# Optimization experiments

Measured on AMD Instinct MI355X. Metric: run time of the kernel, lower is better.

## Reference

```python
import jax, jax.numpy as jnp
import numpy as np

B, T, D, H, HS = 4, 1024, 1024, 16, 64
DW, DA, DG, DV = 64, 64, 128, 32
DM = H * HS  # == D here
EPS = 1e-5
DECAY_C = -0.606531  # -exp(-0.5)


def setup_inputs() -> dict:
    key = jax.random.key(0)
    ks = jax.random.split(key, 24)
    n = lambda k, s: jax.random.normal(k, s, dtype=jnp.float32)
    w = lambda k, s: n(k, s) * (1.0 / np.sqrt(s[0]))
    return dict(
        current=n(ks[0], (B, T, D)),
        prev=n(ks[1], (B, T, D)),
        v_first=n(ks[2], (B, T, DM)),
        rwkvag=jax.random.uniform(ks[3], (6, D), dtype=jnp.float32),
        rw_W=w(ks[4], (D, D)),
        w1=w(ks[5], (D, DW)), w2=w(ks[6], (DW, DM)), w2_b=n(ks[7], (DM,)) * 0.1,
        kw_W=w(ks[8], (D, DM)), vw_W=w(ks[9], (D, DM)),
        a1=w(ks[10], (D, DA)), a2=w(ks[11], (DA, DM)), a2_b=n(ks[12], (DM,)) * 0.1,
        v1=w(ks[13], (D, DV)), v2=w(ks[14], (DV, DM)), v2_b=n(ks[15], (DM,)) * 0.1,
        g1=w(ks[16], (D, DG)), g2=w(ks[17], (DG, DM)), g2_b=n(ks[18], (DM,)) * 0.1,
        k_k=jnp.ones((DM,)), k_a=jax.random.uniform(ks[19], (DM,), dtype=jnp.float32),
        r_k=jnp.ones((DM,)),
        gn_scale=jnp.ones((DM,)), gn_bias=jnp.zeros((DM,)),
        out_W=w(ks[20], (DM, D)),
    )


def _add_heads(x):
    return x.reshape(x.shape[:-1] + (H, HS))


def reference(current, prev, v_first, rwkvag, rw_W, w1, w2, w2_b, kw_W, vw_W,
              a1, a2, a2_b, v1, v2, v2_b, g1, g2, g2_b,
              k_k, k_a, r_k, gn_scale, gn_bias, out_W):
    diff = prev - current
    # per-channel token-shift mixing for the 6 branches: (B,T,6,D)
    x6 = current[..., None, :] + rwkvag * diff[..., None, :]
    xr, xw, xk, xv, xa, xg = (x6[..., i, :] for i in range(6))

    r = xr @ rw_W
    wl = jnp.tanh(xw @ w1) @ w2 + w2_b          # w-LoRA (tanh, bias_post)
    k = xk @ kw_W
    v = xv @ vw_W
    a = jax.nn.sigmoid((xa @ a1) @ a2 + a2_b)   # a-LoRA (bias_post) + sigmoid
    g = jax.nn.sigmoid(xg @ g1) @ g2 + g2_b     # g-LoRA (sigmoid act)

    kk = _add_heads(k * k_k)
    kk = kk / jnp.linalg.norm(kk, axis=-1, keepdims=True)
    k = k * (1.0 + (a - 1.0) * k_a)
    v = v + (v_first - v) * jax.nn.sigmoid((xv @ v1) @ v2 + v2_b)
    wdec = jnp.exp(DECAY_C * jax.nn.sigmoid(wl))  # decay in (exp(-0.6065), 1)

    rk_sum = _add_heads(r * k * r_k).sum(-1, keepdims=True)  # (B,T,H,1)
    rh, wh, kh, vh = _add_heads(r), _add_heads(wdec), _add_heads(k), _add_heads(v)
    at = -kk
    bt = kk * _add_heads(a)

    def step(state, xs):
        rt, wt, ktt, vt, att, btt = xs  # each (B,H,HS)
        sa = jnp.einsum('bhvk,bhk->bhv', state, att)
        state = (state * wt[:, :, None, :]
                 + sa[..., None] * btt[:, :, None, :]
                 + vt[..., None] * ktt[:, :, None, :])
        y = jnp.einsum('bhvk,bhk->bhv', state, rt)
        return state, y

    xs = tuple(jnp.moveaxis(x, 1, 0) for x in (rh, wh, kh, vh, at, bt))
    state0 = jnp.zeros((B, H, HS, HS), dtype=current.dtype)
    state, ys = jax.lax.scan(step, state0, xs)
    out = jnp.moveaxis(ys, 0, 1)  # (B,T,H,HS)

    # GroupNorm with n_head groups (normalize within each head)
    mu = out.mean(-1, keepdims=True)
    var = out.var(-1, keepdims=True)
    outn = (out - mu) * jax.lax.rsqrt(var + EPS)
    outn = outn.reshape(B, T, DM) * gn_scale + gn_bias

    outn = outn + (rk_sum * vh).reshape(B, T, DM)
    y = (outn * g) @ out_W
    return y, state, v_first
```

## Files before the change

kernel.cpp:

```cpp
#include <hip/hip_runtime.h>
#include <math.h>

#define NT 4096
#define DD 1024
#define NH 16
#define HSZ 64
#define GN_EPS 1e-5f
#define DECAY_C -0.606531f

typedef __attribute__((ext_vector_type(8))) short short8;
typedef __attribute__((ext_vector_type(4))) float float4v;

#define GLB(p) ((const __attribute__((address_space(1))) void*)(p))
#define LDS(p) ((__attribute__((address_space(3))) void*)(p))

#define MEMFENCE asm volatile("" ::: "memory")

__device__ __forceinline__ float sigm(float x) { return 1.f / (1.f + __expf(-x)); }

__device__ __forceinline__ unsigned short f2bf(float f) {
    unsigned int u = __float_as_uint(f);
    u = (u + 0x7fffu + ((u >> 16) & 1u)) >> 16;
    return (unsigned short)u;
}
__device__ __forceinline__ float bf2f(unsigned short h) {
    return __uint_as_float(((unsigned int)h) << 16);
}

__device__ __forceinline__ float row_sum16(float x) {
    int t;
    t = __builtin_amdgcn_update_dpp(0, __float_as_int(x), 0x128, 0xF, 0xF, true);
    x += __int_as_float(t);
    t = __builtin_amdgcn_update_dpp(0, __float_as_int(x), 0x124, 0xF, 0xF, true);
    x += __int_as_float(t);
    t = __builtin_amdgcn_update_dpp(0, __float_as_int(x), 0x122, 0xF, 0xF, true);
    x += __int_as_float(t);
    t = __builtin_amdgcn_update_dpp(0, __float_as_int(x), 0x121, 0xF, 0xF, true);
    x += __int_as_float(t);
    return x;
}

__global__ __launch_bounds__(256)
void mix6(const float* __restrict__ cur, const float* __restrict__ prev,
          const float* __restrict__ lam,
          ushort* __restrict__ xrh, ushort* __restrict__ xrl,
          ushort* __restrict__ xwh, ushort* __restrict__ xwl,
          ushort* __restrict__ xkh, ushort* __restrict__ xkl,
          ushort* __restrict__ xvh, ushort* __restrict__ xvl,
          ushort* __restrict__ xah, ushort* __restrict__ xal,
          ushort* __restrict__ xgh, ushort* __restrict__ xgl)
{
    const int tok = blockIdx.x;
    const int d0 = threadIdx.x * 4;
    const size_t base = (size_t)tok * DD + d0;
    float4 c = *(const float4*)(cur + base);
    float4 p = *(const float4*)(prev + base);
    float dx = p.x - c.x, dy = p.y - c.y, dz = p.z - c.z, dw = p.w - c.w;
    ushort* hs[6] = {xrh, xwh, xkh, xvh, xah, xgh};
    ushort* ls[6] = {xrl, xwl, xkl, xvl, xal, xgl};
#pragma unroll
    for (int j = 0; j < 6; j++) {
        float4 l = *(const float4*)(lam + j * DD + d0);
        float m0 = c.x + l.x * dx;
        float m1 = c.y + l.y * dy;
        float m2 = c.z + l.z * dz;
        float m3 = c.w + l.w * dw;
        ushort4 h;
        h.x = f2bf(m0); h.y = f2bf(m1); h.z = f2bf(m2); h.w = f2bf(m3);
        *(ushort4*)(hs[j] + base) = h;
        ushort4 lo;
        lo.x = f2bf(m0 - bf2f(h.x));
        lo.y = f2bf(m1 - bf2f(h.y));
        lo.z = f2bf(m2 - bf2f(h.z));
        lo.w = f2bf(m3 - bf2f(h.w));
        *(ushort4*)(ls[j] + base) = lo;
    }
}

__global__ __launch_bounds__(256)
void transpose_pad(const float* __restrict__ W, ushort* __restrict__ Wh,
                   ushort* __restrict__ Wl, int K, int N)
{
    __shared__ float tile[32][33];
    const int bx = blockIdx.x * 32;
    const int by = blockIdx.y * 32;
    const int tx = threadIdx.x, ty = threadIdx.y;
#pragma unroll
    for (int i = 0; i < 32; i += 8) {
        float v = 0.f;
        if (bx + tx < N) v = W[(size_t)(by + ty + i) * N + bx + tx];
        tile[ty + i][tx] = v;
    }
    __syncthreads();
#pragma unroll
    for (int i = 0; i < 32; i += 8) {
        float v = tile[tx][ty + i];
        ushort h = f2bf(v);
        size_t o = (size_t)(bx + ty + i) * K + by + tx;
        Wh[o] = h;
        if (Wl) Wl[o] = f2bf(v - bf2f(h));
    }
}

#define SWZ(r) (((r) >> 1) & 3)

__global__ __launch_bounds__(256)
void gemm_mega1(const ushort* __restrict__ xrh, const ushort* __restrict__ xrl,
                const ushort* __restrict__ xwh, const ushort* __restrict__ xwl,
                const ushort* __restrict__ xkh, const ushort* __restrict__ xkl,
                const ushort* __restrict__ xvh, const ushort* __restrict__ xvl,
                const ushort* __restrict__ xah, const ushort* __restrict__ xal,
                const ushort* __restrict__ xgh, const ushort* __restrict__ xgl,
                const ushort* __restrict__ Bth, const ushort* __restrict__ Btl,
                float* __restrict__ r_buf, float* __restrict__ k_buf,
                float* __restrict__ v_buf,
                ushort* __restrict__ hwh, ushort* __restrict__ hwl,
                ushort* __restrict__ hah, ushort* __restrict__ hal,
                ushort* __restrict__ hvh, ushort* __restrict__ hvl,
                ushort* __restrict__ hgh, ushort* __restrict__ hgl)
{
    __shared__ ushort As[2][2][128 * 32];
    __shared__ ushort Bs[2][2][128 * 32];
    const int cb = blockIdx.y;
    const ushort* Ah; const ushort* Al;
    if (cb < 8)       { Ah = xrh; Al = xrl; }
    else if (cb < 16) { Ah = xkh; Al = xkl; }
    else if (cb < 24) { Ah = xvh; Al = xvl; }
    else if (cb == 24){ Ah = xwh; Al = xwl; }
    else if (cb == 25){ Ah = xah; Al = xal; }
    else if (cb == 26){ Ah = xvh; Al = xvl; }
    else              { Ah = xgh; Al = xgl; }

    const int tid = threadIdx.x;
    const int rowBase = blockIdx.x * 128;
    const int colBase = cb * 128;
    const int lane = tid & 63;
    const int wave = tid >> 6;
    const int wm = wave >> 1, wn = wave & 1;
    const int m15 = lane & 15, quad = lane >> 4;

    float4v zero4 = {0.f, 0.f, 0.f, 0.f};
    float4v acc[4][4];
#pragma unroll
    for (int i = 0; i < 4; i++)
#pragma unroll
        for (int j = 0; j < 4; j++) acc[i][j] = zero4;

#define STAGE1(kk, bb) do {                                                       \
    const int k0_ = (kk) * 32;                                                    \
    _Pragma("unroll")                                                             \
    for (int i_ = 0; i_ < 2; i_++) {                                              \
        int idx_ = i_ * 256 + tid;                                                \
        int r_ = idx_ >> 2, seg_ = idx_ & 3;                                      \
        int sg_ = seg_ ^ SWZ(r_);       \
        size_t aoff_ = (size_t)(rowBase + r_) * 1024 + k0_ + sg_ * 8;             \
        size_t boff_ = (size_t)(colBase + r_) * 1024 + k0_ + sg_ * 8;             \
        int dst_ = (i_ * 256 + (tid & ~63)) * 8;                                  \
        __builtin_amdgcn_global_load_lds(GLB(Ah + aoff_),  LDS(&As[bb][0][0] + dst_), 16, 0, 0); \
        __builtin_amdgcn_global_load_lds(GLB(Al + aoff_),  LDS(&As[bb][1][0] + dst_), 16, 0, 0); \
        __builtin_amdgcn_global_load_lds(GLB(Bth + boff_), LDS(&Bs[bb][0][0] + dst_), 16, 0, 0); \
        __builtin_amdgcn_global_load_lds(GLB(Btl + boff_), LDS(&Bs[bb][1][0] + dst_), 16, 0, 0); \
    }                                                                             \
} while (0)

    STAGE1(0, 0);
    STAGE1(1, 1);
    asm volatile("s_waitcnt vmcnt(8)" ::: "memory");
    __builtin_amdgcn_s_barrier();
    MEMFENCE;

    for (int kt = 0; kt < 32; kt++) {
        const int buf = kt & 1;

        short8 ah[4], bh[4], al[4], bl[4];
#pragma unroll
        for (int mi = 0; mi < 4; mi++) {
            int ra = wm * 64 + mi * 16 + m15;
            int cs = (quad ^ SWZ(ra)) * 8;
            ah[mi] = *(const short8*)(&As[buf][0][0] + ra * 32 + cs);
            al[mi] = *(const short8*)(&As[buf][1][0] + ra * 32 + cs);
        }
#pragma unroll
        for (int ni = 0; ni < 4; ni++) {
            int rb = wn * 64 + ni * 16 + m15;
            int cs = (quad ^ SWZ(rb)) * 8;
            bh[ni] = *(const short8*)(&Bs[buf][0][0] + rb * 32 + cs);
            bl[ni] = *(const short8*)(&Bs[buf][1][0] + rb * 32 + cs);
        }
#pragma unroll
        for (int mi = 0; mi < 4; mi++)
#pragma unroll
            for (int ni = 0; ni < 4; ni++) {
                acc[mi][ni] = __builtin_amdgcn_mfma_f32_16x16x32_bf16(al[mi], bh[ni], acc[mi][ni], 0, 0, 0);
                acc[mi][ni] = __builtin_amdgcn_mfma_f32_16x16x32_bf16(ah[mi], bl[ni], acc[mi][ni], 0, 0, 0);
                acc[mi][ni] = __builtin_amdgcn_mfma_f32_16x16x32_bf16(ah[mi], bh[ni], acc[mi][ni], 0, 0, 0);
            }

        if (kt == 31) break;

        MEMFENCE;
        __builtin_amdgcn_s_barrier();
        MEMFENCE;
        if (kt < 30) {
            STAGE1(kt + 2, buf);
            asm volatile("s_waitcnt vmcnt(8)" ::: "memory");
        } else {
            asm volatile("s_waitcnt vmcnt(0)" ::: "memory");
        }
        __builtin_amdgcn_s_barrier();
        MEMFENCE;
    }
#undef STAGE1

#pragma unroll
    for (int mi = 0; mi < 4; mi++) {
#pragma unroll
        for (int ni = 0; ni < 4; ni++) {
            int c = wn * 64 + ni * 16 + m15;
#pragma unroll
            for (int rr = 0; rr < 4; rr++) {
                int row = rowBase + wm * 64 + mi * 16 + quad * 4 + rr;
                float v = acc[mi][ni][rr];
                if (cb < 24) {
                    float* dst = (cb < 8) ? r_buf : (cb < 16) ? k_buf : v_buf;
                    int n = (cb & 7) * 128 + c;
                    dst[(size_t)row * 1024 + n] = v;
                } else if (cb == 24) {
                    if (c < 64) {
                        float t = tanhf(v);
                        ushort h = f2bf(t);
                        hwh[(size_t)row * 64 + c] = h;
                        hwl[(size_t)row * 64 + c] = f2bf(t - bf2f(h));
                    }
                } else if (cb == 25) {
                    if (c < 64) {
                        ushort h = f2bf(v);
                        hah[(size_t)row * 64 + c] = h;
                        hal[(size_t)row * 64 + c] = f2bf(v - bf2f(h));
                    }
                } else if (cb == 26) {
                    if (c < 32) {
                        ushort h = f2bf(v);
                        hvh[(size_t)row * 32 + c] = h;
                        hvl[(size_t)row * 32 + c] = f2bf(v - bf2f(h));
                    }
                } else {
                    float t = sigm(v);
                    ushort h = f2bf(t);
                    hgh[(size_t)row * 128 + c] = h;
                    hgl[(size_t)row * 128 + c] = f2bf(t - bf2f(h));
                }
            }
        }
    }
}

__global__ __launch_bounds__(256)
void gemm_mega2(const ushort* __restrict__ hwh, const ushort* __restrict__ hwl,
                const ushort* __restrict__ hah, const ushort* __restrict__ hal,
                const ushort* __restrict__ hvh, const ushort* __restrict__ hvl,
                const ushort* __restrict__ hgh, const ushort* __restrict__ hgl,
                const ushort* __restrict__ w2Th, const ushort* __restrict__ w2Tl,
                const ushort* __restrict__ a2Th, const ushort* __restrict__ a2Tl,
                const ushort* __restrict__ v2Th, const ushort* __restrict__ v2Tl,
                const ushort* __restrict__ g2Th, const ushort* __restrict__ g2Tl,
                const float* __restrict__ w2_b, const float* __restrict__ a2_b,
                const float* __restrict__ v2_b, const float* __restrict__ g2_b,
                float* __restrict__ w_buf, float* __restrict__ a_buf,
                float* __restrict__ vg_buf, float* __restrict__ g_buf)
{
    __shared__ ushort AsH[128 * 32];
    __shared__ ushort BsH[128 * 32];
    __shared__ ushort AsL[128 * 32];
    __shared__ ushort BsL[128 * 32];
    const int cb = blockIdx.y;
    const int seg = cb >> 3;
    const int K = (seg == 2) ? 32 : (seg == 3) ? 128 : 64;
    const ushort *Ah, *Al, *Bh, *Bl;
    const float* bias;
    float* outp;
    if (seg == 0) { Ah = hwh; Al = hwl; Bh = w2Th; Bl = w2Tl; bias = w2_b; outp = w_buf; }
    else if (seg == 1) { Ah = hah; Al = hal; Bh = a2Th; Bl = a2Tl; bias = a2_b; outp = a_buf; }
    else if (seg == 2) { Ah = hvh; Al = hvl; Bh = v2Th; Bl = v2Tl; bias = v2_b; outp = vg_buf; }
    else { Ah = hgh; Al = hgl; Bh = g2Th; Bl = g2Tl; bias = g2_b; outp = g_buf; }

    const int tid = threadIdx.x;
    const int rowBase = blockIdx.x * 128;
    const int colBase = (cb & 7) * 128;
    const int lane = tid & 63;
    const int wave = tid >> 6;
    const int wm = wave >> 1, wn = wave & 1;
    const int m15 = lane & 15, quad = lane >> 4;

    float4v zero4 = {0.f, 0.f, 0.f, 0.f};
    float4v acc[4][4];
#pragma unroll
    for (int i = 0; i < 4; i++)
#pragma unroll
        for (int j = 0; j < 4; j++) acc[i][j] = zero4;

    for (int k0 = 0; k0 < K; k0 += 32) {
#pragma unroll
        for (int i = 0; i < 2; i++) {
            int idx = i * 256 + tid;
            int r = idx >> 2, s8 = idx & 3;
            int sg = s8 ^ SWZ(r);
            size_t aoff = (size_t)(rowBase + r) * K + k0 + sg * 8;
            size_t boff = (size_t)(colBase + r) * K + k0 + sg * 8;
            int dst = (i * 256 + (tid & ~63)) * 8;
            __builtin_amdgcn_global_load_lds(GLB(Ah + aoff), LDS(AsH + dst), 16, 0, 0);
            __builtin_amdgcn_global_load_lds(GLB(Bh + boff), LDS(BsH + dst), 16, 0, 0);
            __builtin_amdgcn_global_load_lds(GLB(Al + aoff), LDS(AsL + dst), 16, 0, 0);
            __builtin_amdgcn_global_load_lds(GLB(Bl + boff), LDS(BsL + dst), 16, 0, 0);
        }
        __syncthreads();
        short8 ah[4], bh[4], al[4], bl[4];
#pragma unroll
        for (int mi = 0; mi < 4; mi++) {
            int ra = wm * 64 + mi * 16 + m15;
            int cs = (quad ^ SWZ(ra)) * 8;
            ah[mi] = *(const short8*)(AsH + ra * 32 + cs);
            al[mi] = *(const short8*)(AsL + ra * 32 + cs);
        }
#pragma unroll
        for (int ni = 0; ni < 4; ni++) {
            int rb = wn * 64 + ni * 16 + m15;
            int cs = (quad ^ SWZ(rb)) * 8;
            bh[ni] = *(const short8*)(BsH + rb * 32 + cs);
            bl[ni] = *(const short8*)(BsL + rb * 32 + cs);
        }
#pragma unroll
        for (int mi = 0; mi < 4; mi++)
#pragma unroll
            for (int ni = 0; ni < 4; ni++) {
                acc[mi][ni] = __builtin_amdgcn_mfma_f32_16x16x32_bf16(al[mi], bh[ni], acc[mi][ni], 0, 0, 0);
                acc[mi][ni] = __builtin_amdgcn_mfma_f32_16x16x32_bf16(ah[mi], bl[ni], acc[mi][ni], 0, 0, 0);
                acc[mi][ni] = __builtin_amdgcn_mfma_f32_16x16x32_bf16(ah[mi], bh[ni], acc[mi][ni], 0, 0, 0);
            }
        __syncthreads();
    }

#pragma unroll
    for (int mi = 0; mi < 4; mi++) {
#pragma unroll
        for (int ni = 0; ni < 4; ni++) {
            int col = colBase + wn * 64 + ni * 16 + m15;
            float bv = bias[col];
#pragma unroll
            for (int rr = 0; rr < 4; rr++) {
                int row = rowBase + wm * 64 + mi * 16 + quad * 4 + rr;
                float v = acc[mi][ni][rr] + bv;
                if (seg == 1 || seg == 2) v = sigm(v);
                outp[(size_t)row * 1024 + col] = v;
            }
        }
    }
}

__global__ __launch_bounds__(256)
void gemm_bf16s(const ushort* __restrict__ Ah, const ushort* __restrict__ Bh,
                float* __restrict__ outF, int N, int K)
{
    __shared__ ushort As2[2][128 * 32];
    __shared__ ushort Bs2[2][128 * 32];
    const int tid = threadIdx.x;
    const int rowBase = blockIdx.x * 128;
    const int colBase = blockIdx.y * 128;
    const int lane = tid & 63;
    const int wave = tid >> 6;
    const int wm = wave >> 1, wn = wave & 1;
    const int m15 = lane & 15, quad = lane >> 4;

    float4v zero4 = {0.f, 0.f, 0.f, 0.f};
    float4v acc[4][4];
#pragma unroll
    for (int i = 0; i < 4; i++)
#pragma unroll
        for (int j = 0; j < 4; j++) acc[i][j] = zero4;

#define STAGE3(kk, bb) do {                                                       \
    const int k0_ = (kk) * 32;                                                    \
    _Pragma("unroll")                                                             \
    for (int i_ = 0; i_ < 2; i_++) {                                              \
        int idx_ = i_ * 256 + tid;                                                \
        int r_ = idx_ >> 2, seg_ = idx_ & 3;                                      \
        int sg_ = seg_ ^ SWZ(r_);                                                 \
        size_t aoff_ = (size_t)(rowBase + r_) * K + k0_ + sg_ * 8;                \
        size_t boff_ = (size_t)(colBase + r_) * K + k0_ + sg_ * 8;                \
        int dst_ = (i_ * 256 + (tid & ~63)) * 8;                                  \
        __builtin_amdgcn_global_load_lds(GLB(Ah + aoff_), LDS(&As2[bb][0] + dst_), 16, 0, 0); \
        __builtin_amdgcn_global_load_lds(GLB(Bh + boff_), LDS(&Bs2[bb][0] + dst_), 16, 0, 0); \
    }                                                                             \
} while (0)

    const int nk = K >> 5;
    STAGE3(0, 0);
    __syncthreads();

    for (int kt = 0; kt < nk; kt++) {
        const int buf = kt & 1;
        if (kt < nk - 1) STAGE3(kt + 1, buf ^ 1);
        short8 ah[4], bh[4];
#pragma unroll
        for (int mi = 0; mi < 4; mi++) {
            int ra = wm * 64 + mi * 16 + m15;
            ah[mi] = *(const short8*)(&As2[buf][0] + ra * 32 + (quad ^ SWZ(ra)) * 8);
        }
#pragma unroll
        for (int ni = 0; ni < 4; ni++) {
            int rb = wn * 64 + ni * 16 + m15;
            bh[ni] = *(const short8*)(&Bs2[buf][0] + rb * 32 + (quad ^ SWZ(rb)) * 8);
        }
#pragma unroll
        for (int mi = 0; mi < 4; mi++)
#pragma unroll
            for (int ni = 0; ni < 4; ni++)
                acc[mi][ni] = __builtin_amdgcn_mfma_f32_16x16x32_bf16(ah[mi], bh[ni], acc[mi][ni], 0, 0, 0);
        __syncthreads();
    }
#undef STAGE3

#pragma unroll
    for (int mi = 0; mi < 4; mi++) {
#pragma unroll
        for (int ni = 0; ni < 4; ni++) {
            int col = colBase + wn * 64 + ni * 16 + m15;
#pragma unroll
            for (int rr = 0; rr < 4; rr++) {
                int row = rowBase + wm * 64 + mi * 16 + quad * 4 + rr;
                outF[(size_t)row * N + col] = acc[mi][ni][rr];
            }
        }
    }
}

__global__ __launch_bounds__(256)
void elemwise1(const float* __restrict__ r_buf, float* __restrict__ wl_buf,
               float* __restrict__ k_buf, float* __restrict__ v_buf,
               float* __restrict__ kkn_buf, const float* __restrict__ a_buf,
               const float* __restrict__ vg_buf, const float* __restrict__ vfirst,
               const float* __restrict__ kkw, const float* __restrict__ kaw,
               const float* __restrict__ rkw, float* __restrict__ rk_sum)
{
    const int tok = blockIdx.x;
    const int tid = threadIdx.x;
    const int d0 = tid * 4;
    const size_t base = (size_t)tok * DD + d0;

    float4 k0 = *(const float4*)(k_buf + base);
    float4 a4 = *(const float4*)(a_buf + base);
    float4 wl = *(const float4*)(wl_buf + base);
    float4 v0 = *(const float4*)(v_buf + base);
    float4 vg = *(const float4*)(vg_buf + base);
    float4 vf = *(const float4*)(vfirst + base);
    float4 r4 = *(const float4*)(r_buf + base);
    float4 kkc = *(const float4*)(kkw + d0);
    float4 kac = *(const float4*)(kaw + d0);
    float4 rkc = *(const float4*)(rkw + d0);

    float kk0 = k0.x * kkc.x, kk1 = k0.y * kkc.y, kk2 = k0.z * kkc.z, kk3 = k0.w * kkc.w;
    float ss = kk0 * kk0 + kk1 * kk1 + kk2 * kk2 + kk3 * kk3;
    ss += __shfl_xor(ss, 1); ss += __shfl_xor(ss, 2);
    ss += __shfl_xor(ss, 4); ss += __shfl_xor(ss, 8);
    float rn = rsqrtf(ss);
    float4 kkn = { kk0 * rn, kk1 * rn, kk2 * rn, kk3 * rn };
    *(float4*)(kkn_buf + base) = kkn;

    float4 kf;
    kf.x = k0.x * (1.f + (a4.x - 1.f) * kac.x);
    kf.y = k0.y * (1.f + (a4.y - 1.f) * kac.y);
    kf.z = k0.z * (1.f + (a4.z - 1.f) * kac.z);
    kf.w = k0.w * (1.f + (a4.w - 1.f) * kac.w);
    *(float4*)(k_buf + base) = kf;

    float rk = r4.x * kf.x * rkc.x + r4.y * kf.y * rkc.y + r4.z * kf.z * rkc.z + r4.w * kf.w * rkc.w;
    rk += __shfl_xor(rk, 1); rk += __shfl_xor(rk, 2);
    rk += __shfl_xor(rk, 4); rk += __shfl_xor(rk, 8);
    if ((tid & 15) == 0) rk_sum[(size_t)tok * NH + (tid >> 4)] = rk;

    float4 vfin;
    vfin.x = v0.x + (vf.x - v0.x) * vg.x;
    vfin.y = v0.y + (vf.y - v0.y) * vg.y;
    vfin.z = v0.z + (vf.z - v0.z) * vg.z;
    vfin.w = v0.w + (vf.w - v0.w) * vg.w;
    *(float4*)(v_buf + base) = vfin;

    float4 wd;
    wd.x = __expf(DECAY_C * sigm(wl.x));
    wd.y = __expf(DECAY_C * sigm(wl.y));
    wd.z = __expf(DECAY_C * sigm(wl.z));
    wd.w = __expf(DECAY_C * sigm(wl.w));
    *(float4*)(wl_buf + base) = wd;
}

__global__ __launch_bounds__(256, 1)
void scan_kernel(const float* __restrict__ r_buf, const float* __restrict__ w_buf,
                 const float* __restrict__ k_buf, const float* __restrict__ kkn_buf,
                 const float* __restrict__ a_buf, const float* __restrict__ v_buf,
                 float* __restrict__ out_scan, float* __restrict__ state_out)
{
    __shared__ float vecJ[2][5][16][64];
    __shared__ float vbuf2[2][16][16];
    __shared__ float ypart[2][16][16][16];
    const int bh = blockIdx.x;
    const int rg = blockIdx.y;
    const int b = bh >> 4, h = bh & 15;
    const int tid = threadIdx.x;
    const int row = tid >> 4, l16 = tid & 15;
    const int lofs = l16 * 4;
    const int rowbase = rg * 16;
    const size_t tok0 = ((size_t)b * 1024) * DD + h * HSZ;
    float s0 = 0.f, s1 = 0.f, s2 = 0.f, s3 = 0.f;

#define STAGE(cc, bb) do {                                                        \
    const int tt_ = tid >> 4;                                                     \
    const int dd4_ = (tid & 15) * 4;                                              \
    size_t gofs_ = tok0 + (size_t)((cc) * 16 + tt_) * DD + dd4_;                  \
    float* db_ = &vecJ[bb][0][0][0] + ((tid >> 6) << 8);                          \
    __builtin_amdgcn_global_load_lds(GLB(r_buf + gofs_),   LDS(db_),        16, 0, 0); \
    __builtin_amdgcn_global_load_lds(GLB(w_buf + gofs_),   LDS(db_ + 1024), 16, 0, 0); \
    __builtin_amdgcn_global_load_lds(GLB(k_buf + gofs_),   LDS(db_ + 2048), 16, 0, 0); \
    __builtin_amdgcn_global_load_lds(GLB(kkn_buf + gofs_), LDS(db_ + 3072), 16, 0, 0); \
    __builtin_amdgcn_global_load_lds(GLB(a_buf + gofs_),   LDS(db_ + 4096), 16, 0, 0); \
    if (tid < 64) {                                                               \
        size_t vofs_ = tok0 + (size_t)((cc) * 16 + (tid >> 2)) * DD + rowbase + (tid & 3) * 4; \
        __builtin_amdgcn_global_load_lds(GLB(v_buf + vofs_), LDS(&vbuf2[bb][0][0]), 16, 0, 0); \
    }                                                                             \
} while (0)

#define LD_TOK(P, tt) do {                                                        \
    P##r = *(const float4*)(vb + (tt) * 64 + lofs);                               \
    P##w = *(const float4*)(vb + 1024 + (tt) * 64 + lofs);                        \
    P##k = *(const float4*)(vb + 2048 + (tt) * 64 + lofs);                        \
    P##q = *(const float4*)(vb + 3072 + (tt) * 64 + lofs);                        \
    P##a = *(const float4*)(vb + 4096 + (tt) * 64 + lofs);                        \
    P##v = vbp[(tt) * 16 + row];                                                  \
} while (0)

#define STEP(P, tt) do {                                                          \
    float sa_ = P##q.x * s0;                                                      \
    sa_ = fmaf(P##q.y, s1, sa_);                                                  \
    sa_ = fmaf(P##q.z, s2, sa_);                                                  \
    sa_ = fmaf(P##q.w, s3, sa_);                                                  \
    sa_ = row_sum16(sa_);                                                         \
    float n0_ = P##q.x * P##a.x, n1_ = P##q.y * P##a.y;                           \
    float n2_ = P##q.z * P##a.z, n3_ = P##q.w * P##a.w;                           \
    float b0_ = fmaf(s0, P##w.x, P##v * P##k.x);                                  \
    float b1_ = fmaf(s1, P##w.y, P##v * P##k.y);                                  \
    float b2_ = fmaf(s2, P##w.z, P##v * P##k.z);                                  \
    float b3_ = fmaf(s3, P##w.w, P##v * P##k.w);                                  \
    s0 = fmaf(sa_, -n0_, b0_);                                                    \
    s1 = fmaf(sa_, -n1_, b1_);                                                    \
    s2 = fmaf(sa_, -n2_, b2_);                                                    \
    s3 = fmaf(sa_, -n3_, b3_);                                                    \
    float yp_ = P##r.x * s0;                                                      \
    yp_ = fmaf(P##r.y, s1, yp_);                                                  \
    yp_ = fmaf(P##r.z, s2, yp_);                                                  \
    yp_ = fmaf(P##r.w, s3, yp_);                                                  \
    ypart[buf][tt][row][l16] = yp_;                                               \
} while (0)

    STAGE(0, 0);
    __syncthreads();

    for (int c = 0; c < 64; c++) {
        const int buf = c & 1;
        if (c < 63) STAGE(c + 1, buf ^ 1);
        const float* vb  = &vecJ[buf][0][0][0];
        const float* vbp = &vbuf2[buf][0][0];
        float4 Ar, Aw, Ak, Aq, Aa; float Av;
        float4 Br, Bw, Bk, Bq, Ba; float Bv;
        float4 Cr, Cw, Ck, Cq, Ca; float Cv;
        float4 Dr, Dw, Dk, Dq, Da; float Dv;
        LD_TOK(A, 0); LD_TOK(B, 1); LD_TOK(C, 2);
#pragma unroll
        for (int i4 = 0; i4 < 4; i4++) {
            LD_TOK(D, 4 * i4 + 3);
            STEP(A, 4 * i4);
            if (4 * i4 + 4 < 16) LD_TOK(A, 4 * i4 + 4);
            STEP(B, 4 * i4 + 1);
            if (4 * i4 + 5 < 16) LD_TOK(B, 4 * i4 + 5);
            STEP(C, 4 * i4 + 2);
            if (4 * i4 + 6 < 16) LD_TOK(C, 4 * i4 + 6);
            STEP(D, 4 * i4 + 3);
        }
        __syncthreads();
        {
            const int t_ = tid >> 4, r_ = tid & 15;
            const float* yp = &ypart[buf][t_][r_][0];
            float4 y0 = *(const float4*)(yp);
            float4 y1 = *(const float4*)(yp + 4);
            float4 y2 = *(const float4*)(yp + 8);
            float4 y3 = *(const float4*)(yp + 12);
            float ys = ((y0.x + y0.y) + (y0.z + y0.w)) + ((y1.x + y1.y) + (y1.z + y1.w))
                     + ((y2.x + y2.y) + (y2.z + y2.w)) + ((y3.x + y3.y) + (y3.z + y3.w));
            out_scan[tok0 + (size_t)(c * 16 + t_) * DD + rowbase + r_] = ys;
        }
    }

#undef STAGE
#undef LD_TOK
#undef STEP

    float* so = state_out + ((size_t)(b * NH + h) * HSZ + rowbase + row) * HSZ + l16 * 4;
    float4 sv = {s0, s1, s2, s3};
    *(float4*)so = sv;
}

__global__ __launch_bounds__(256)
void elemwise2(const float* __restrict__ out_scan, const float* __restrict__ rk_sum,
               const float* __restrict__ v_buf, const float* __restrict__ g_buf,
               const float* __restrict__ gscale, const float* __restrict__ gbias,
               ushort* __restrict__ z_buf)
{
    const int tok = blockIdx.x;
    const int tid = threadIdx.x;
    const int d0 = tid * 4;
    const size_t base = (size_t)tok * DD + d0;

    float4 o = *(const float4*)(out_scan + base);
    float sm = o.x + o.y + o.z + o.w;
    float ss = o.x * o.x + o.y * o.y + o.z * o.z + o.w * o.w;
    sm += __shfl_xor(sm, 1); sm += __shfl_xor(sm, 2);
    sm += __shfl_xor(sm, 4); sm += __shfl_xor(sm, 8);
    ss += __shfl_xor(ss, 1); ss += __shfl_xor(ss, 2);
    ss += __shfl_xor(ss, 4); ss += __shfl_xor(ss, 8);
    float mu = sm * (1.f / 64.f);
    float var = ss * (1.f / 64.f) - mu * mu;
    float rs = rsqrtf(var + GN_EPS);
    float rk = rk_sum[(size_t)tok * NH + (tid >> 4)];

    float4 v4 = *(const float4*)(v_buf + base);
    float4 g4 = *(const float4*)(g_buf + base);
    float4 gs = *(const float4*)(gscale + d0);
    float4 gb = *(const float4*)(gbias + d0);
    ushort4 z;
    z.x = f2bf(((o.x - mu) * rs * gs.x + gb.x + rk * v4.x) * g4.x);
    z.y = f2bf(((o.y - mu) * rs * gs.y + gb.y + rk * v4.y) * g4.y);
    z.z = f2bf(((o.z - mu) * rs * gs.z + gb.z + rk * v4.z) * g4.z);
    z.w = f2bf(((o.w - mu) * rs * gs.w + gb.w + rk * v4.w) * g4.w);
    *(ushort4*)(z_buf + base) = z;
}

extern "C" void kernel_launch(void* const* d_in, const int* in_sizes, int n_in,
                              void* d_out, int out_size, void* d_ws, size_t ws_size,
                              hipStream_t stream) {
    const float* cur    = (const float*)d_in[0];
    const float* prev   = (const float*)d_in[1];
    const float* vfirst = (const float*)d_in[2];
    const float* rwkvag = (const float*)d_in[3];
    const float* rw_W   = (const float*)d_in[4];
    const float* w1     = (const float*)d_in[5];
    const float* w2     = (const float*)d_in[6];
    const float* w2_b   = (const float*)d_in[7];
    const float* kw_W   = (const float*)d_in[8];
    const float* vw_W   = (const float*)d_in[9];
    const float* a1     = (const float*)d_in[10];
    const float* a2     = (const float*)d_in[11];
    const float* a2_b   = (const float*)d_in[12];
    const float* v1     = (const float*)d_in[13];
    const float* v2     = (const float*)d_in[14];
    const float* v2_b   = (const float*)d_in[15];
    const float* g1     = (const float*)d_in[16];
    const float* g2     = (const float*)d_in[17];
    const float* g2_b   = (const float*)d_in[18];
    const float* k_k    = (const float*)d_in[19];
    const float* k_a    = (const float*)d_in[20];
    const float* r_k    = (const float*)d_in[21];
    const float* gn_s   = (const float*)d_in[22];
    const float* gn_b   = (const float*)d_in[23];
    const float* out_W  = (const float*)d_in[24];

    float* out = (float*)d_out;
    float* y_out = out;
    float* state_out = out + (size_t)NT * DD;
    float* vf_out = state_out + (size_t)4 * NH * HSZ * HSZ;

    float* p = (float*)d_ws;
    const size_t big = (size_t)NT * DD;
    const size_t half = big / 2;
    float* r_buf = p;   p += big;
    float* k_buf = p;   p += big;
    float* v_buf = p;   p += big;
    float* xreg = p;
    ushort* xrh = (ushort*)(xreg);            ushort* xrl = (ushort*)(xreg + half);
    ushort* xwh = (ushort*)(xreg + 2*half);   ushort* xwl = (ushort*)(xreg + 3*half);
    ushort* xkh = (ushort*)(xreg + 4*half);   ushort* xkl = (ushort*)(xreg + 5*half);
    ushort* xvh = (ushort*)(xreg + 6*half);   ushort* xvl = (ushort*)(xreg + 7*half);
    ushort* xah = (ushort*)(xreg + 8*half);   ushort* xal = (ushort*)(xreg + 9*half);
    ushort* xgh = (ushort*)(xreg + 10*half);  ushort* xgl = (ushort*)(xreg + 11*half);
    p += 12 * half;
    float* w_buf   = xreg + 0 * half;
    float* a_buf   = xreg + 2 * half;
    float* vg_buf  = xreg + 4 * half;
    float* os_buf  = vg_buf;
    float* g_buf   = xreg + 6 * half;
    float* kkn_buf = xreg + 8 * half;
    float* btreg = p;
    ushort* Bth = (ushort*)btreg;
    ushort* Btl = (ushort*)(btreg + 1835008);
    p += 2 * 1835008;
    ushort* z_bf  = (ushort*)btreg;
    ushort* outTh = (ushort*)(btreg + 2097152);
    ushort* w2Th = (ushort*)p; p += 32768; ushort* w2Tl = (ushort*)p; p += 32768;
    ushort* a2Th = (ushort*)p; p += 32768; ushort* a2Tl = (ushort*)p; p += 32768;
    ushort* v2Th = (ushort*)p; p += 16384; ushort* v2Tl = (ushort*)p; p += 16384;
    ushort* g2Th = (ushort*)p; p += 65536; ushort* g2Tl = (ushort*)p; p += 65536;
    ushort* hwh = (ushort*)p; p += 131072; ushort* hwl = (ushort*)p; p += 131072;
    ushort* hah = (ushort*)p; p += 131072; ushort* hal = (ushort*)p; p += 131072;
    ushort* hvh = (ushort*)p; p += 65536;  ushort* hvl = (ushort*)p; p += 65536;
    ushort* hgh = (ushort*)p; p += 262144; ushort* hgl = (ushort*)p; p += 262144;
    float* rks_buf = p;        p += 65536;

    dim3 blk(256);
    dim3 t32x8(32, 8);

    transpose_pad<<<dim3(32, 32), t32x8, 0, stream>>>(rw_W, Bth + (size_t)0 * 1024,    Btl + (size_t)0 * 1024,    1024, 1024);
    transpose_pad<<<dim3(32, 32), t32x8, 0, stream>>>(kw_W, Bth + (size_t)1024 * 1024, Btl + (size_t)1024 * 1024, 1024, 1024);
    transpose_pad<<<dim3(32, 32), t32x8, 0, stream>>>(vw_W, Bth + (size_t)2048 * 1024, Btl + (size_t)2048 * 1024, 1024, 1024);
    transpose_pad<<<dim3(4, 32), t32x8, 0, stream>>>(w1, Bth + (size_t)3072 * 1024, Btl + (size_t)3072 * 1024, 1024, 64);
    transpose_pad<<<dim3(4, 32), t32x8, 0, stream>>>(a1, Bth + (size_t)3200 * 1024, Btl + (size_t)3200 * 1024, 1024, 64);
    transpose_pad<<<dim3(4, 32), t32x8, 0, stream>>>(v1, Bth + (size_t)3328 * 1024, Btl + (size_t)3328 * 1024, 1024, 32);
    transpose_pad<<<dim3(4, 32), t32x8, 0, stream>>>(g1, Bth + (size_t)3456 * 1024, Btl + (size_t)3456 * 1024, 1024, 128);
    transpose_pad<<<dim3(32, 2), t32x8, 0, stream>>>(w2, w2Th, w2Tl, 64, 1024);
    transpose_pad<<<dim3(32, 2), t32x8, 0, stream>>>(a2, a2Th, a2Tl, 64, 1024);
    transpose_pad<<<dim3(32, 1), t32x8, 0, stream>>>(v2, v2Th, v2Tl, 32, 1024);
    transpose_pad<<<dim3(32, 4), t32x8, 0, stream>>>(g2, g2Th, g2Tl, 128, 1024);

    mix6<<<NT, blk, 0, stream>>>(cur, prev, rwkvag,
                                 xrh, xrl, xwh, xwl, xkh, xkl,
                                 xvh, xvl, xah, xal, xgh, xgl);

    gemm_mega1<<<dim3(32, 28), blk, 0, stream>>>(
        xrh, xrl, xwh, xwl, xkh, xkl, xvh, xvl, xah, xal, xgh, xgl,
        Bth, Btl, r_buf, k_buf, v_buf,
        hwh, hwl, hah, hal, hvh, hvl, hgh, hgl);

    transpose_pad<<<dim3(32, 32), t32x8, 0, stream>>>(out_W, outTh, nullptr, 1024, 1024);

    gemm_mega2<<<dim3(32, 32), blk, 0, stream>>>(
        hwh, hwl, hah, hal, hvh, hvl, hgh, hgl,
        w2Th, w2Tl, a2Th, a2Tl, v2Th, v2Tl, g2Th, g2Tl,
        w2_b, a2_b, v2_b, g2_b,
        w_buf, a_buf, vg_buf, g_buf);

    elemwise1<<<NT, blk, 0, stream>>>(r_buf, w_buf, k_buf, v_buf, kkn_buf, a_buf,
                                      vg_buf, vfirst, k_k, k_a, r_k, rks_buf);

    scan_kernel<<<dim3(64, 4), blk, 0, stream>>>(r_buf, w_buf, k_buf, kkn_buf, a_buf, v_buf,
                                                 os_buf, state_out);

    elemwise2<<<NT, blk, 0, stream>>>(os_buf, rks_buf, v_buf, g_buf, gn_s, gn_b, z_bf);

    gemm_bf16s<<<dim3(32, 8), blk, 0, stream>>>(z_bf, outTh, y_out, 1024, 1024);

    hipMemcpyAsync(vf_out, vfirst, (size_t)NT * DD * sizeof(float),
                   hipMemcpyDeviceToDevice, stream);
}
```

Baseline: 516.8 us.

## Split scan into single-wave blocks of four state rows each

The recurrence scan now launches 1024 blocks of 64 threads, each owning four rows of a head's 64x64 state, instead of 256 blocks of 256 threads owning sixteen rows. Each wave stages the r/w/k/kk/a chunks itself into LDS, prefetches v from global into registers, and reduces the output with a row shuffle-sum written directly, dropping the shared ypart buffer. This spreads the serial scan over more CUs and avoids the cross-wave output reduction. In exchange, each block redundantly loads the full key-side vectors, so global and LDS traffic per state row grows fourfold.

```diff
diff --git a/kernel.cpp b/kernel.cpp
--- a/kernel.cpp
+++ b/kernel.cpp
@@ -493,38 +493,34 @@
     *(float4*)(wl_buf + base) = wd;
 }
 
-__global__ __launch_bounds__(256, 1)
+__global__ __launch_bounds__(64)
 void scan_kernel(const float* __restrict__ r_buf, const float* __restrict__ w_buf,
                  const float* __restrict__ k_buf, const float* __restrict__ kkn_buf,
                  const float* __restrict__ a_buf, const float* __restrict__ v_buf,
                  float* __restrict__ out_scan, float* __restrict__ state_out)
 {
     __shared__ float vecJ[2][5][16][64];
-    __shared__ float vbuf2[2][16][16];
-    __shared__ float ypart[2][16][16][16];
     const int bh = blockIdx.x;
     const int rg = blockIdx.y;
     const int b = bh >> 4, h = bh & 15;
     const int tid = threadIdx.x;
-    const int row = tid >> 4, l16 = tid & 15;
+    const int row = tid >> 4;
+    const int l16 = tid & 15;
     const int lofs = l16 * 4;
-    const int rowbase = rg * 16;
+    const int rowbase = rg * 4;
     const size_t tok0 = ((size_t)b * 1024) * DD + h * HSZ;
     float s0 = 0.f, s1 = 0.f, s2 = 0.f, s3 = 0.f;
 
+    const float* bs[5] = {r_buf, w_buf, k_buf, kkn_buf, a_buf};
+
 #define STAGE(cc, bb) do {                                                        \
-    const int tt_ = tid >> 4;                                                     \
-    const int dd4_ = (tid & 15) * 4;                                              \
-    size_t gofs_ = tok0 + (size_t)((cc) * 16 + tt_) * DD + dd4_;                  \
-    float* db_ = &vecJ[bb][0][0][0] + ((tid >> 6) << 8);                          \
-    __builtin_amdgcn_global_load_lds(GLB(r_buf + gofs_),   LDS(db_),        16, 0, 0); \
-    __builtin_amdgcn_global_load_lds(GLB(w_buf + gofs_),   LDS(db_ + 1024), 16, 0, 0); \
-    __builtin_amdgcn_global_load_lds(GLB(k_buf + gofs_),   LDS(db_ + 2048), 16, 0, 0); \
-    __builtin_amdgcn_global_load_lds(GLB(kkn_buf + gofs_), LDS(db_ + 3072), 16, 0, 0); \
-    __builtin_amdgcn_global_load_lds(GLB(a_buf + gofs_),   LDS(db_ + 4096), 16, 0, 0); \
-    if (tid < 64) {                                                               \
-        size_t vofs_ = tok0 + (size_t)((cc) * 16 + (tid >> 2)) * DD + rowbase + (tid & 3) * 4; \
-        __builtin_amdgcn_global_load_lds(GLB(v_buf + vofs_), LDS(&vbuf2[bb][0][0]), 16, 0, 0); \
+    _Pragma("unroll")                                                             \
+    for (int i_ = 0; i_ < 20; i_++) {                                             \
+        const float* src_ = bs[i_ >> 2];                                          \
+        int t_ = (i_ & 3) * 4 + (tid >> 4);                                       \
+        size_t g_ = tok0 + (size_t)((cc) * 16 + t_) * DD + lofs;                  \
+        __builtin_amdgcn_global_load_lds(GLB(src_ + g_),                          \
+            LDS(&vecJ[bb][0][0][0] + i_ * 256), 16, 0, 0);                        \
     }                                                                             \
 } while (0)
 
@@ -534,7 +530,6 @@
     P##k = *(const float4*)(vb + 2048 + (tt) * 64 + lofs);                        \
     P##q = *(const float4*)(vb + 3072 + (tt) * 64 + lofs);                        \
     P##a = *(const float4*)(vb + 4096 + (tt) * 64 + lofs);                        \
-    P##v = vbp[(tt) * 16 + row];                                                  \
 } while (0)
 
 #define STEP(P, tt) do {                                                          \
@@ -543,59 +538,55 @@
     sa_ = fmaf(P##q.z, s2, sa_);                                                  \
     sa_ = fmaf(P##q.w, s3, sa_);                                                  \
     sa_ = row_sum16(sa_);                                                         \
+    float vv_ = vc[tt];                                                           \
     float n0_ = P##q.x * P##a.x, n1_ = P##q.y * P##a.y;                           \
     float n2_ = P##q.z * P##a.z, n3_ = P##q.w * P##a.w;                           \
-    float b0_ = fmaf(s0, P##w.x, P##v * P##k.x);                                  \
-    float b1_ = fmaf(s1, P##w.y, P##v * P##k.y);                                  \
-    float b2_ = fmaf(s2, P##w.z, P##v * P##k.z);                                  \
-    float b3_ = fmaf(s3, P##w.w, P##v * P##k.w);                                  \
+    float b0_ = fmaf(s0, P##w.x, vv_ * P##k.x);                                   \
+    float b1_ = fmaf(s1, P##w.y, vv_ * P##k.y);                                   \
+    float b2_ = fmaf(s2, P##w.z, vv_ * P##k.z);                                   \
+    float b3_ = fmaf(s3, P##w.w, vv_ * P##k.w);                                   \
     s0 = fmaf(sa_, -n0_, b0_);                                                    \
     s1 = fmaf(sa_, -n1_, b1_);                                                    \
     s2 = fmaf(sa_, -n2_, b2_);                                                    \
     s3 = fmaf(sa_, -n3_, b3_);                                                    \
-    float yp_ = P##r.x * s0;                                                      \
-    yp_ = fmaf(P##r.y, s1, yp_);                                                  \
-    yp_ = fmaf(P##r.z, s2, yp_);                                                  \
-    yp_ = fmaf(P##r.w, s3, yp_);                                                  \
-    ypart[buf][tt][row][l16] = yp_;                                               \
+    float y_ = P##r.x * s0;                                                       \
+    y_ = fmaf(P##r.y, s1, y_);                                                    \
+    y_ = fmaf(P##r.z, s2, y_);                                                    \
+    y_ = fmaf(P##r.w, s3, y_);                                                    \
+    y_ = row_sum16(y_);                                                           \
+    if (l16 == 0)                                                                 \
+        out_scan[tok0 + (size_t)((c) * 16 + (tt)) * DD + rowbase + row] = y_;     \
 } while (0)
 
+    float vc[16], vn[16];
+#pragma unroll
+    for (int t = 0; t < 16; t++)
+        vc[t] = v_buf[tok0 + (size_t)t * DD + rowbase + row];
     STAGE(0, 0);
     __syncthreads();
 
     for (int c = 0; c < 64; c++) {
         const int buf = c & 1;
-        if (c < 63) STAGE(c + 1, buf ^ 1);
-        const float* vb  = &vecJ[buf][0][0][0];
-        const float* vbp = &vbuf2[buf][0][0];
-        float4 Ar, Aw, Ak, Aq, Aa; float Av;
-        float4 Br, Bw, Bk, Bq, Ba; float Bv;
-        float4 Cr, Cw, Ck, Cq, Ca; float Cv;
-        float4 Dr, Dw, Dk, Dq, Da; float Dv;
-        LD_TOK(A, 0); LD_TOK(B, 1); LD_TOK(C, 2);
-#pragma unroll
-        for (int i4 = 0; i4 < 4; i4++) {
-            LD_TOK(D, 4 * i4 + 3);
-            STEP(A, 4 * i4);
-            if (4 * i4 + 4 < 16) LD_TOK(A, 4 * i4 + 4);
-            STEP(B, 4 * i4 + 1);
-            if (4 * i4 + 5 < 16) LD_TOK(B, 4 * i4 + 5);
-            STEP(C, 4 * i4 + 2);
-            if (4 * i4 + 6 < 16) LD_TOK(C, 4 * i4 + 6);
-            STEP(D, 4 * i4 + 3);
+        if (c < 63) {
+            STAGE(c + 1, buf ^ 1);
+#pragma unroll
+            for (int t = 0; t < 16; t++)
+                vn[t] = v_buf[tok0 + (size_t)((c + 1) * 16 + t) * DD + rowbase + row];
+        }
+        const float* vb = &vecJ[buf][0][0][0];
+        float4 Ar, Aw, Ak, Aq, Aa;
+        float4 Br, Bw, Bk, Bq, Ba;
+        LD_TOK(A, 0);
+#pragma unroll
+        for (int tp = 0; tp < 8; tp++) {
+            LD_TOK(B, 2 * tp + 1);
+            STEP(A, 2 * tp);
+            if (tp < 7) LD_TOK(A, 2 * tp + 2);
+            STEP(B, 2 * tp + 1);
         }
         __syncthreads();
-        {
-            const int t_ = tid >> 4, r_ = tid & 15;
-            const float* yp = &ypart[buf][t_][r_][0];
-            float4 y0 = *(const float4*)(yp);
-            float4 y1 = *(const float4*)(yp + 4);
-            float4 y2 = *(const float4*)(yp + 8);
-            float4 y3 = *(const float4*)(yp + 12);
-            float ys = ((y0.x + y0.y) + (y0.z + y0.w)) + ((y1.x + y1.y) + (y1.z + y1.w))
-                     + ((y2.x + y2.y) + (y2.z + y2.w)) + ((y3.x + y3.y) + (y3.z + y3.w));
-            out_scan[tok0 + (size_t)(c * 16 + t_) * DD + rowbase + r_] = ys;
-        }
+#pragma unroll
+        for (int t = 0; t < 16; t++) vc[t] = vn[t];
     }
 
 #undef STAGE
@@ -747,8 +738,8 @@
     elemwise1<<<NT, blk, 0, stream>>>(r_buf, w_buf, k_buf, v_buf, kkn_buf, a_buf,
                                       vg_buf, vfirst, k_k, k_a, r_k, rks_buf);
 
-    scan_kernel<<<dim3(64, 4), blk, 0, stream>>>(r_buf, w_buf, k_buf, kkn_buf, a_buf, v_buf,
-                                                 os_buf, state_out);
+    scan_kernel<<<dim3(64, 16), dim3(64), 0, stream>>>(r_buf, w_buf, k_buf, kkn_buf, a_buf, v_buf,
+                                                       os_buf, state_out);
 
     elemwise2<<<NT, blk, 0, stream>>>(os_buf, rks_buf, v_buf, g_buf, gn_s, gn_b, z_bf);
 
```

Result: slower. 558.8 us (+8.1%).
